# Performance work log

Measured on AMD Instinct MI355X. Metric: run time of the kernel, lower is better.

The kernel has to match this reference:

```python
import jax, jax.numpy as jnp
import numpy as np

# Static config derived from img size 144 (min spatial dim > 128 branch):
SCALES = [9, 18, 36]            # kernel sizes (cubic)
WEIGHTS = [0.1, 0.3, 0.6]       # kernel weight ratios
DILATIONS = [2, 2, 2]
STRIDES = [max((k + 1) // 4, 1) for k in SCALES]  # [2, 4, 9]
EPS = 1e-5


def _box_sum(x, k, stride, dil):
    # Local sum over a dilated k^3 window, valid padding (matches F.conv3d
    # with an all-ones [1,1,k,k,k] kernel).
    kern = jnp.ones((1, 1, k, k, k), dtype=x.dtype)
    return jax.lax.conv_general_dilated(
        x, kern,
        window_strides=(stride,) * 3,
        padding='VALID',
        rhs_dilation=(dil,) * 3,
        dimension_numbers=('NCDHW', 'OIDHW', 'NCDHW'))


def setup_inputs() -> dict:
    key = jax.random.key(0)
    k1, k2 = jax.random.split(key)
    shape = (4, 1, 144, 144, 144)
    return {
        'input': jax.random.normal(k1, shape, dtype=jnp.float32),
        'target': jax.random.normal(k2, shape, dtype=jnp.float32),
    }


def reference(input, target):
    B = input.shape[0]
    input_2 = input * input
    target_2 = target * target
    input_target = input * target
    lncc_total = jnp.float32(0.0)
    for k, w, dil, st in zip(SCALES, WEIGHTS, DILATIONS, STRIDES):
        i_sum = _box_sum(input, k, st, dil).reshape(B, -1)
        t_sum = _box_sum(target, k, st, dil).reshape(B, -1)
        i2_sum = _box_sum(input_2, k, st, dil).reshape(B, -1)
        t2_sum = _box_sum(target_2, k, st, dil).reshape(B, -1)
        it_sum = _box_sum(input_target, k, st, dil).reshape(B, -1)
        numel = float(k ** 3)
        i_mean = i_sum / numel
        t_mean = t_sum / numel
        cross = it_sum - t_mean * i_sum - i_mean * t_sum + t_mean * i_mean * numel
        i_var = i2_sum - 2.0 * i_mean * i_sum + i_mean * i_mean * numel
        t_var = t2_sum - 2.0 * t_mean * t_sum + t_mean * t_mean * numel
        lncc = (cross * cross) / (i_var * t_var + EPS)
        lncc_total = lncc_total + w * (1.0 - lncc.mean())
    return lncc_total * B
```

## Files before the change

kernel.cpp:

```cpp
#include <hip/hip_runtime.h>


constexpr int BATCH = 4;
constexpr int DIM   = 144;
constexpr int NROWS = BATCH * DIM * DIM;
constexpr float EPS = 1e-5f;

constexpr int N1C  = NROWS * 9;
constexpr int N2Ae = BATCH * 72 * 64 * 64;
constexpr int N2Be = BATCH * 72 * 28 * 28;
constexpr int N2C  = BATCH * DIM * 9 * 9;


__device__ __forceinline__ float lncc_val(const float s[5], float inv_numel) {
    float cross = s[4] - s[0] * s[1] * inv_numel;
    float ivar  = s[2] - s[0] * s[0] * inv_numel;
    float tvar  = s[3] - s[1] * s[1] * inv_numel;
    return (cross * cross) / (ivar * tvar + EPS);
}

__device__ __forceinline__ void block_reduce_store(float acc, float* slot) {
    #pragma unroll
    for (int off = 32; off > 0; off >>= 1) acc += __shfl_down(acc, off, 64);
    __shared__ float sm[4];
    int lane = threadIdx.x & 63, wid = threadIdx.x >> 6;
    if (lane == 0) sm[wid] = acc;
    __syncthreads();
    if (threadIdx.x == 0) *slot = sm[0] + sm[1] + sm[2] + sm[3];
}


__device__ void aXY_body(int blk, const float* __restrict__ in,
                         const float* __restrict__ tg,
                         float* __restrict__ b2a, float* xs)
{
    const int p  = blk >> 2;
    const int c  = blk & 3;
    const int b  = p / 72;
    const int ez = p % 72;
    const int xo0 = c * 16;
    const size_t gpl = (size_t)(b * DIM + 2 * ez) * (DIM * DIM);
    const int t = threadIdx.x;

    for (int i = t; i < 576; i += 256) {
        int yp = i >> 3, dp = i & 7;
        int dx0 = dp * 2;
        int e0  = xo0 + dx0;
        const float* rowa = in + gpl + (size_t)(2 * yp) * DIM;
        const float* rowb = tg + gpl + (size_t)(2 * yp) * DIM;
        const float4* ga = (const float4*)rowa + (e0 >> 1);
        const float4* gb = (const float4*)rowb + (e0 >> 1);
        float ea[10], eb[10];
        #pragma unroll
        for (int k = 0; k < 5; ++k) {
            float4 A = ga[k]; ea[2 * k] = A.x; ea[2 * k + 1] = A.z;
            float4 B = gb[k]; eb[2 * k] = B.x; eb[2 * k + 1] = B.z;
        }
        float* xr = &xs[yp * 82 + dx0];
        #pragma unroll
        for (int q = 0; q < 5; ++q) {
            float2 sq; sq.x = 0.f; sq.y = 0.f;
            #pragma unroll
            for (int j = 0; j < 9; ++j) {
                float a0 = ea[j],     b0 = eb[j];
                float a1 = ea[j + 1], b1 = eb[j + 1];
                float v0, v1;
                if (q == 0)      { v0 = a0;      v1 = a1; }
                else if (q == 1) { v0 = b0;      v1 = b1; }
                else if (q == 2) { v0 = a0 * a0; v1 = a1 * a1; }
                else if (q == 3) { v0 = b0 * b0; v1 = b1 * b1; }
                else             { v0 = a0 * b0; v1 = a1 * b1; }
                sq.x += v0; sq.y += v1;
            }
            *(float2*)&xr[q * 16] = sq;
        }
    }
    __syncthreads();

    if (t < 160) {
        int dp = t & 7;
        int ch = (t >> 3) & 3;
        int q  = t >> 5;
        int dx0 = 2 * dp, yo0 = ch * 16;
        const float2* xp2 = (const float2*)xs + ((q * 16 + dx0) >> 1);
        float2 s; s.x = 0.f; s.y = 0.f;
        #pragma unroll
        for (int j = 0; j < 9; ++j) {
            float2 v = xp2[(yo0 + j) * 41];
            s.x += v.x; s.y += v.y;
        }
        float2* ob = (float2*)(b2a + (size_t)q * N2Ae
                               + ((size_t)p * 64 + yo0) * 64 + xo0 + dx0);
        ob[0] = s;
        #pragma unroll
        for (int i2 = 1; i2 < 16; ++i2) {
            float2 vn = xp2[(yo0 + i2 + 8) * 41];
            float2 vo = xp2[(yo0 + i2 - 1) * 41];
            s.x += vn.x - vo.x; s.y += vn.y - vo.y;
            ob[(size_t)i2 * 32] = s;
        }
    }
}

constexpr int CXROWS   = 24;
constexpr int CXSTRIDE = 292;

__device__ void cX_body(int blk, const float* __restrict__ in,
                        const float* __restrict__ tg,
                        float* __restrict__ b1c, float* lv)
{
    const int t = threadIdx.x;
    const int row0 = blk * CXROWS;
    const float4* gin = (const float4*)(in + (size_t)row0 * DIM);
    const float4* gtg = (const float4*)(tg + (size_t)row0 * DIM);
    for (int i4 = t; i4 < CXROWS * 36; i4 += 256) {
        int rr = i4 / 36, k = i4 % 36;
        float4 A = gin[i4], B = gtg[i4];
        float4* d = (float4*)&lv[rr * CXSTRIDE + k * 8];
        float4 w0; w0.x = A.x; w0.y = B.x; w0.z = A.y; w0.w = B.y;
        float4 w1; w1.x = A.z; w1.y = B.z; w1.z = A.w; w1.w = B.w;
        d[0] = w0; d[1] = w1;
    }
    __syncthreads();
    if (t < CXROWS * 9) {
        int rr = t / 9, xo = t % 9;
        const float2* pp = (const float2*)&lv[rr * CXSTRIDE] + xo * 9;
        float s0 = 0.f, s1 = 0.f, s2 = 0.f, s3 = 0.f, s4 = 0.f;
        #pragma unroll
        for (int j = 0; j < 36; ++j) {
            float2 ab = pp[2 * j];
            float a = ab.x, bb = ab.y;
            s0 += a; s1 += bb; s2 += a * a; s3 += bb * bb; s4 += a * bb;
        }
        int o = (row0 + rr) * 9 + xo;
        b1c[o] = s0; b1c[N1C + o] = s1; b1c[2 * N1C + o] = s2;
        b1c[3 * N1C + o] = s3; b1c[4 * N1C + o] = s4;
    }
}

constexpr int B_AXY = BATCH * 72 * 4;
constexpr int B_CX  = NROWS / CXROWS;
constexpr int SM1   = CXROWS * CXSTRIDE;

__global__ __launch_bounds__(256) void k1(const float* __restrict__ in,
                                          const float* __restrict__ tg,
                                          float* __restrict__ b2a,
                                          float* __restrict__ b1c)
{
    __shared__ float smem[SM1];
    int blk = blockIdx.x;
    if (blk < B_AXY) aXY_body(blk, in, tg, b2a, smem);
    else             cX_body(blk - B_AXY, in, tg, b1c, smem);
}


__device__ __forceinline__ void bXY_body(int tid, const float* __restrict__ b2a,
                                         float* __restrict__ b2b)
{
    const int total = BATCH * 72 * 28 * 14;
    if (tid >= total) return;
    int px = tid % 14;
    int yo = (tid / 14) % 28;
    int p  = tid / 392;
    const float* ib = b2a + (size_t)p * 4096;
    int r0 = 2 * yo * 64, r1 = r0 + 9 * 64;
    #pragma unroll
    for (int q = 0; q < 5; ++q) {
        const float* pq = ib + (size_t)q * N2Ae;
        const float4* row0 = (const float4*)(pq + r0);
        const float4* row1 = (const float4*)(pq + r1);
        float4 a0 = row0[px], b0 = row0[px + 2];
        float4 a1 = row1[px], b1 = row1[px + 2];
        float2 o;
        o.x = a0.x + b0.y + a1.x + b1.y;
        o.y = a0.z + b0.w + a1.z + b1.w;
        *(float2*)(b2b + (size_t)q * N2Be + (size_t)p * 784 + yo * 28 + 2 * px) = o;
    }
}

__device__ __forceinline__ void cY_body(int tid, const float* __restrict__ b1c,
                                        float* __restrict__ b2c)
{
    const int total = BATCH * DIM * 9 * 9 * 8;
    if (tid >= total) return;
    int sp   = tid & 7;
    int rest = tid >> 3;
    int xo = rest % 9;
    int yo = (rest / 9) % 9;
    int bz = rest / 81;
    const float* base = b1c + (size_t)bz * DIM * 9 + xo;

    float s[5] = {0.f, 0.f, 0.f, 0.f, 0.f};
    #pragma unroll
    for (int j = 0; j < 36; ++j) {
        if ((j & 7) == sp) {
            int y = 9 * yo + 2 * j;
            #pragma unroll
            for (int q = 0; q < 5; ++q) s[q] += base[(size_t)q * N1C + y * 9];
        }
    }
    #pragma unroll
    for (int off = 1; off < 8; off <<= 1) {
        #pragma unroll
        for (int q = 0; q < 5; ++q) s[q] += __shfl_xor(s[q], off, 64);
    }
    if (sp == 0) {
        float* ob = b2c + (size_t)bz * 81 + yo * 9 + xo;
        #pragma unroll
        for (int q = 0; q < 5; ++q) ob[(size_t)q * N2C] = s[q];
    }
}

constexpr int B_BXY = (BATCH * 72 * 28 * 14) / 256;
constexpr int B_CY  = (BATCH * DIM * 9 * 9 * 8) / 256;

__global__ __launch_bounds__(256) void k2a(const float* __restrict__ b2a,
                                           const float* __restrict__ b1c,
                                           float* __restrict__ b2b,
                                           float* __restrict__ b2c)
{
    int blk = blockIdx.x;
    if (blk < B_BXY) bXY_body(blk * 256 + threadIdx.x, b2a, b2b);
    else             cY_body((blk - B_BXY) * 256 + threadIdx.x, b1c, b2c);
}


__device__ __forceinline__ void aZ_body(int blk, const float* __restrict__ b2a,
                                        float* __restrict__ pA)
{
    int tid = blk * 256 + threadIdx.x;
    float acc = 0.f;
    {
        int xo = tid & 63;
        int yo = (tid >> 6) & 63;
        int ch = (tid >> 12) & 7;
        int b  = tid >> 15;
        const int zo0 = ch * 8;
        const int OO = 64 * 64;
        const float* base = b2a + (size_t)b * 72 * OO + yo * 64 + xo;

        float s[5] = {0.f, 0.f, 0.f, 0.f, 0.f};
        #pragma unroll
        for (int j = 0; j < 9; ++j) {
            #pragma unroll
            for (int q = 0; q < 5; ++q)
                s[q] += base[(size_t)q * N2Ae + (zo0 + j) * OO];
        }
        acc += lncc_val(s, 1.0f / 729.0f);
        #pragma unroll
        for (int i = 1; i < 8; ++i) {
            #pragma unroll
            for (int q = 0; q < 5; ++q)
                s[q] += base[(size_t)q * N2Ae + (zo0 + i + 8) * OO]
                      - base[(size_t)q * N2Ae + (zo0 + i - 1) * OO];
            acc += lncc_val(s, 1.0f / 729.0f);
        }
    }
    block_reduce_store(acc, pA + blk);
}

__device__ __forceinline__ void bZ_body(int blk, const float* __restrict__ b2b,
                                        float* __restrict__ pB)
{
    int tid = blk * 256 + threadIdx.x;
    float acc = 0.f;
    {
        int sp   = tid & 7;
        int rest = tid >> 3;
        int px = rest % 14;
        int yo = (rest / 14) % 28;
        int zo = (rest / 392) % 28;
        int b  = rest / 10976;
        const int OO = 784;
        const float* base = b2b + (size_t)b * 72 * OO + yo * 28 + 2 * px;

        float sx[5] = {0.f, 0.f, 0.f, 0.f, 0.f};
        float sy[5] = {0.f, 0.f, 0.f, 0.f, 0.f};
        #pragma unroll
        for (int j = 0; j < 18; ++j) {
            if ((j & 7) == sp) {
                #pragma unroll
                for (int q = 0; q < 5; ++q) {
                    float2 v = *(const float2*)(base + (size_t)q * N2Be
                                                + (2 * zo + j) * OO);
                    sx[q] += v.x; sy[q] += v.y;
                }
            }
        }
        #pragma unroll
        for (int off = 1; off < 8; off <<= 1) {
            #pragma unroll
            for (int q = 0; q < 5; ++q) {
                sx[q] += __shfl_xor(sx[q], off, 64);
                sy[q] += __shfl_xor(sy[q], off, 64);
            }
        }
        if (sp == 0)
            acc = lncc_val(sx, 1.0f / 5832.0f) + lncc_val(sy, 1.0f / 5832.0f);
    }
    block_reduce_store(acc, pB + blk);
}

__device__ __forceinline__ void cZ_body(int blk, const float* __restrict__ b2c,
                                        float* __restrict__ pC)
{
    int tid = blk * 256 + threadIdx.x;
    const int total = BATCH * 9 * 9 * 9 * 16;
    float acc = 0.f;
    if (tid < total) {
        int sp   = tid & 15;
        int rest = tid >> 4;
        int xo = rest % 9;
        int yo = (rest / 9) % 9;
        int zo = (rest / 81) % 9;
        int b  = rest / 729;
        const int OO = 81;
        const float* base = b2c + (size_t)b * DIM * OO + yo * 9 + xo;

        float s[5] = {0.f, 0.f, 0.f, 0.f, 0.f};
        #pragma unroll
        for (int j = 0; j < 36; ++j) {
            if ((j & 15) == sp) {
                int z = 9 * zo + 2 * j;
                #pragma unroll
                for (int q = 0; q < 5; ++q) s[q] += base[(size_t)q * N2C + z * OO];
            }
        }
        #pragma unroll
        for (int off = 1; off < 16; off <<= 1) {
            #pragma unroll
            for (int q = 0; q < 5; ++q) s[q] += __shfl_xor(s[q], off, 64);
        }
        if (sp == 0) acc = lncc_val(s, 1.0f / 46656.0f);
    }
    block_reduce_store(acc, pC + blk);
}

constexpr int B_AZ = (BATCH * 8 * 64 * 64) / 256;
constexpr int B_BZ = (BATCH * 28 * 28 * 14 * 8) / 256;
constexpr int B_CZ = (BATCH * 9 * 9 * 9 * 16 + 255) / 256;

__global__ __launch_bounds__(256) void k2b(const float* __restrict__ b2a,
                                           const float* __restrict__ b2b,
                                           const float* __restrict__ b2c,
                                           float* __restrict__ pA,
                                           float* __restrict__ pB,
                                           float* __restrict__ pC)
{
    int blk = blockIdx.x;
    if (blk < B_AZ)             aZ_body(blk, b2a, pA);
    else if (blk < B_AZ + B_BZ) bZ_body(blk - B_AZ, b2b, pB);
    else                        cZ_body(blk - B_AZ - B_BZ, b2c, pC);
}


__global__ __launch_bounds__(256) void k4(const float* __restrict__ pA,
                                          const float* __restrict__ pB,
                                          const float* __restrict__ pC,
                                          float* __restrict__ out)
{
    const int t = threadIdx.x;
    float sA = 0.f, sB = 0.f, sC = 0.f;
    for (int i = t; i < B_AZ; i += 256) sA += pA[i];
    for (int i = t; i < B_BZ; i += 256) sB += pB[i];
    for (int i = t; i < B_CZ; i += 256) sC += pC[i];
    float s = (0.1f / 262144.0f) * sA + (0.3f / 21952.0f) * sB
            + (0.6f / 729.0f) * sC;
    #pragma unroll
    for (int off = 32; off > 0; off >>= 1) s += __shfl_down(s, off, 64);
    __shared__ float sm[4];
    int lane = t & 63, wid = t >> 6;
    if (lane == 0) sm[wid] = s;
    __syncthreads();
    if (t == 0) out[0] = 4.0f - (sm[0] + sm[1] + sm[2] + sm[3]);
}

extern "C" void kernel_launch(void* const* d_in, const int* in_sizes, int n_in,
                              void* d_out, int out_size, void* d_ws, size_t ws_size,
                              hipStream_t stream) {
    const float* input  = (const float*)d_in[0];
    const float* target = (const float*)d_in[1];
    float* out = (float*)d_out;

    float* b2a = (float*)d_ws;
    float* b1c = b2a + (size_t)5 * N2Ae;
    float* b2b = b1c + (size_t)5 * N1C;
    float* b2c = b2b + (size_t)5 * N2Be;
    float* pA  = b2c + (size_t)5 * N2C;
    float* pB  = pA + B_AZ;
    float* pC  = pB + B_BZ;

    k1<<<B_AXY + B_CX, 256, 0, stream>>>(input, target, b2a, b1c);
    k2a<<<B_BXY + B_CY, 256, 0, stream>>>(b2a, b1c, b2b, b2c);
    k2b<<<B_AZ + B_BZ + B_CZ, 256, 0, stream>>>(b2a, b2b, b2c, pA, pB, pC);
    k4<<<1, 256, 0, stream>>>(pA, pB, pC, out);
}
```

Measured before the change: 88.10 us.

## Fuse scale-C X and Y passes per plane and regroup stages across kernels

```diff
diff --git a/kernel.cpp b/kernel.cpp
--- a/kernel.cpp
+++ b/kernel.cpp
@@ -3,10 +3,8 @@
 
 constexpr int BATCH = 4;
 constexpr int DIM   = 144;
-constexpr int NROWS = BATCH * DIM * DIM;
 constexpr float EPS = 1e-5f;
 
-constexpr int N1C  = NROWS * 9;
 constexpr int N2Ae = BATCH * 72 * 64 * 64;
 constexpr int N2Be = BATCH * 72 * 28 * 28;
 constexpr int N2C  = BATCH * DIM * 9 * 9;
@@ -102,57 +100,94 @@
     }
 }
 
-constexpr int CXROWS   = 24;
-constexpr int CXSTRIDE = 292;
-
-__device__ void cX_body(int blk, const float* __restrict__ in,
-                        const float* __restrict__ tg,
-                        float* __restrict__ b1c, float* lv)
-{
+
+__device__ void cXY_body(int blk, const float* __restrict__ in,
+                         const float* __restrict__ tg,
+                         float* __restrict__ b2c, float* xs)
+{
+    const size_t gpl = (size_t)blk * (DIM * DIM);
     const int t = threadIdx.x;
-    const int row0 = blk * CXROWS;
-    const float4* gin = (const float4*)(in + (size_t)row0 * DIM);
-    const float4* gtg = (const float4*)(tg + (size_t)row0 * DIM);
-    for (int i4 = t; i4 < CXROWS * 36; i4 += 256) {
-        int rr = i4 / 36, k = i4 % 36;
-        float4 A = gin[i4], B = gtg[i4];
-        float4* d = (float4*)&lv[rr * CXSTRIDE + k * 8];
-        float4 w0; w0.x = A.x; w0.y = B.x; w0.z = A.y; w0.w = B.y;
-        float4 w1; w1.x = A.z; w1.y = B.z; w1.z = A.w; w1.w = B.w;
-        d[0] = w0; d[1] = w1;
+
+    for (int i = t; i < 144 * 9; i += 256) {
+        int y = i / 9, xo = i % 9;
+        int x0 = 9 * xo;
+        const float2* ra = (const float2*)(in + gpl + (size_t)y * DIM) + (x0 >> 1);
+        const float2* rb = (const float2*)(tg + gpl + (size_t)y * DIM) + (x0 >> 1);
+        const bool odd = (x0 & 1) != 0;
+        float s0 = 0.f, s1 = 0.f, s2 = 0.f, s3 = 0.f, s4 = 0.f;
+        #pragma unroll
+        for (int j = 0; j < 36; ++j) {
+            float2 va = ra[j], vb = rb[j];
+            float a  = odd ? va.y : va.x;
+            float bb = odd ? vb.y : vb.x;
+            s0 += a; s1 += bb; s2 += a * a; s3 += bb * bb; s4 += a * bb;
+        }
+        float* d = &xs[y * 48 + xo * 5];
+        d[0] = s0; d[1] = s1; d[2] = s2; d[3] = s3; d[4] = s4;
     }
     __syncthreads();
-    if (t < CXROWS * 9) {
-        int rr = t / 9, xo = t % 9;
-        const float2* pp = (const float2*)&lv[rr * CXSTRIDE] + xo * 9;
-        float s0 = 0.f, s1 = 0.f, s2 = 0.f, s3 = 0.f, s4 = 0.f;
-        #pragma unroll
-        for (int j = 0; j < 36; ++j) {
-            float2 ab = pp[2 * j];
-            float a = ab.x, bb = ab.y;
-            s0 += a; s1 += bb; s2 += a * a; s3 += bb * bb; s4 += a * bb;
-        }
-        int o = (row0 + rr) * 9 + xo;
-        b1c[o] = s0; b1c[N1C + o] = s1; b1c[2 * N1C + o] = s2;
-        b1c[3 * N1C + o] = s3; b1c[4 * N1C + o] = s4;
+
+    for (int i = t; i < 405; i += 256) {
+        int q  = i % 5;
+        int xo = (i / 5) % 9;
+        int yo = i / 45;
+        float s = 0.f;
+        #pragma unroll
+        for (int j = 0; j < 36; ++j)
+            s += xs[(9 * yo + 2 * j) * 48 + xo * 5 + q];
+        b2c[(size_t)q * N2C + ((size_t)blk * 9 + yo) * 9 + xo] = s;
     }
 }
 
 constexpr int B_AXY = BATCH * 72 * 4;
-constexpr int B_CX  = NROWS / CXROWS;
-constexpr int SM1   = CXROWS * CXSTRIDE;
+constexpr int B_CXY = BATCH * DIM;
+constexpr int SM1   = 144 * 48;
 
 __global__ __launch_bounds__(256) void k1(const float* __restrict__ in,
                                           const float* __restrict__ tg,
                                           float* __restrict__ b2a,
-                                          float* __restrict__ b1c)
+                                          float* __restrict__ b2c)
 {
     __shared__ float smem[SM1];
     int blk = blockIdx.x;
     if (blk < B_AXY) aXY_body(blk, in, tg, b2a, smem);
-    else             cX_body(blk - B_AXY, in, tg, b1c, smem);
-}
-
+    else             cXY_body(blk - B_AXY, in, tg, b2c, smem);
+}
+
+
+__device__ __forceinline__ void aZ_body(int blk, const float* __restrict__ b2a,
+                                        float* __restrict__ pA)
+{
+    int tid = blk * 256 + threadIdx.x;
+    float acc = 0.f;
+    {
+        int xo = tid & 63;
+        int yo = (tid >> 6) & 63;
+        int ch = (tid >> 12) & 15;
+        int b  = tid >> 16;
+        const int zo0 = ch * 4;
+        const int OO = 64 * 64;
+        const float* base = b2a + (size_t)b * 72 * OO + yo * 64 + xo;
+
+        float s[5] = {0.f, 0.f, 0.f, 0.f, 0.f};
+        #pragma unroll
+        for (int j = 0; j < 9; ++j) {
+            #pragma unroll
+            for (int q = 0; q < 5; ++q)
+                s[q] += base[(size_t)q * N2Ae + (zo0 + j) * OO];
+        }
+        acc += lncc_val(s, 1.0f / 729.0f);
+        #pragma unroll
+        for (int i = 1; i < 4; ++i) {
+            #pragma unroll
+            for (int q = 0; q < 5; ++q)
+                s[q] += base[(size_t)q * N2Ae + (zo0 + i + 8) * OO]
+                      - base[(size_t)q * N2Ae + (zo0 + i - 1) * OO];
+            acc += lncc_val(s, 1.0f / 729.0f);
+        }
+    }
+    block_reduce_store(acc, pA + blk);
+}
 
 __device__ __forceinline__ void bXY_body(int tid, const float* __restrict__ b2a,
                                          float* __restrict__ b2b)
@@ -178,129 +213,6 @@
     }
 }
 
-__device__ __forceinline__ void cY_body(int tid, const float* __restrict__ b1c,
-                                        float* __restrict__ b2c)
-{
-    const int total = BATCH * DIM * 9 * 9 * 8;
-    if (tid >= total) return;
-    int sp   = tid & 7;
-    int rest = tid >> 3;
-    int xo = rest % 9;
-    int yo = (rest / 9) % 9;
-    int bz = rest / 81;
-    const float* base = b1c + (size_t)bz * DIM * 9 + xo;
-
-    float s[5] = {0.f, 0.f, 0.f, 0.f, 0.f};
-    #pragma unroll
-    for (int j = 0; j < 36; ++j) {
-        if ((j & 7) == sp) {
-            int y = 9 * yo + 2 * j;
-            #pragma unroll
-            for (int q = 0; q < 5; ++q) s[q] += base[(size_t)q * N1C + y * 9];
-        }
-    }
-    #pragma unroll
-    for (int off = 1; off < 8; off <<= 1) {
-        #pragma unroll
-        for (int q = 0; q < 5; ++q) s[q] += __shfl_xor(s[q], off, 64);
-    }
-    if (sp == 0) {
-        float* ob = b2c + (size_t)bz * 81 + yo * 9 + xo;
-        #pragma unroll
-        for (int q = 0; q < 5; ++q) ob[(size_t)q * N2C] = s[q];
-    }
-}
-
-constexpr int B_BXY = (BATCH * 72 * 28 * 14) / 256;
-constexpr int B_CY  = (BATCH * DIM * 9 * 9 * 8) / 256;
-
-__global__ __launch_bounds__(256) void k2a(const float* __restrict__ b2a,
-                                           const float* __restrict__ b1c,
-                                           float* __restrict__ b2b,
-                                           float* __restrict__ b2c)
-{
-    int blk = blockIdx.x;
-    if (blk < B_BXY) bXY_body(blk * 256 + threadIdx.x, b2a, b2b);
-    else             cY_body((blk - B_BXY) * 256 + threadIdx.x, b1c, b2c);
-}
-
-
-__device__ __forceinline__ void aZ_body(int blk, const float* __restrict__ b2a,
-                                        float* __restrict__ pA)
-{
-    int tid = blk * 256 + threadIdx.x;
-    float acc = 0.f;
-    {
-        int xo = tid & 63;
-        int yo = (tid >> 6) & 63;
-        int ch = (tid >> 12) & 7;
-        int b  = tid >> 15;
-        const int zo0 = ch * 8;
-        const int OO = 64 * 64;
-        const float* base = b2a + (size_t)b * 72 * OO + yo * 64 + xo;
-
-        float s[5] = {0.f, 0.f, 0.f, 0.f, 0.f};
-        #pragma unroll
-        for (int j = 0; j < 9; ++j) {
-            #pragma unroll
-            for (int q = 0; q < 5; ++q)
-                s[q] += base[(size_t)q * N2Ae + (zo0 + j) * OO];
-        }
-        acc += lncc_val(s, 1.0f / 729.0f);
-        #pragma unroll
-        for (int i = 1; i < 8; ++i) {
-            #pragma unroll
-            for (int q = 0; q < 5; ++q)
-                s[q] += base[(size_t)q * N2Ae + (zo0 + i + 8) * OO]
-                      - base[(size_t)q * N2Ae + (zo0 + i - 1) * OO];
-            acc += lncc_val(s, 1.0f / 729.0f);
-        }
-    }
-    block_reduce_store(acc, pA + blk);
-}
-
-__device__ __forceinline__ void bZ_body(int blk, const float* __restrict__ b2b,
-                                        float* __restrict__ pB)
-{
-    int tid = blk * 256 + threadIdx.x;
-    float acc = 0.f;
-    {
-        int sp   = tid & 7;
-        int rest = tid >> 3;
-        int px = rest % 14;
-        int yo = (rest / 14) % 28;
-        int zo = (rest / 392) % 28;
-        int b  = rest / 10976;
-        const int OO = 784;
-        const float* base = b2b + (size_t)b * 72 * OO + yo * 28 + 2 * px;
-
-        float sx[5] = {0.f, 0.f, 0.f, 0.f, 0.f};
-        float sy[5] = {0.f, 0.f, 0.f, 0.f, 0.f};
-        #pragma unroll
-        for (int j = 0; j < 18; ++j) {
-            if ((j & 7) == sp) {
-                #pragma unroll
-                for (int q = 0; q < 5; ++q) {
-                    float2 v = *(const float2*)(base + (size_t)q * N2Be
-                                                + (2 * zo + j) * OO);
-                    sx[q] += v.x; sy[q] += v.y;
-                }
-            }
-        }
-        #pragma unroll
-        for (int off = 1; off < 8; off <<= 1) {
-            #pragma unroll
-            for (int q = 0; q < 5; ++q) {
-                sx[q] += __shfl_xor(sx[q], off, 64);
-                sy[q] += __shfl_xor(sy[q], off, 64);
-            }
-        }
-        if (sp == 0)
-            acc = lncc_val(sx, 1.0f / 5832.0f) + lncc_val(sy, 1.0f / 5832.0f);
-    }
-    block_reduce_store(acc, pB + blk);
-}
-
 __device__ __forceinline__ void cZ_body(int blk, const float* __restrict__ b2c,
                                         float* __restrict__ pC)
 {
@@ -336,21 +248,71 @@
     block_reduce_store(acc, pC + blk);
 }
 
-constexpr int B_AZ = (BATCH * 8 * 64 * 64) / 256;
+constexpr int B_AZ  = (BATCH * 16 * 64 * 64) / 256;
+constexpr int B_BXY = (BATCH * 72 * 28 * 14) / 256;
+constexpr int B_CZ  = (BATCH * 9 * 9 * 9 * 16 + 255) / 256;
+
+__global__ __launch_bounds__(256) void k2(const float* __restrict__ b2a,
+                                          const float* __restrict__ b2c,
+                                          float* __restrict__ b2b,
+                                          float* __restrict__ pA,
+                                          float* __restrict__ pC)
+{
+    int blk = blockIdx.x;
+    if (blk < B_AZ)              aZ_body(blk, b2a, pA);
+    else if (blk < B_AZ + B_BXY) bXY_body((blk - B_AZ) * 256 + threadIdx.x, b2a, b2b);
+    else                         cZ_body(blk - B_AZ - B_BXY, b2c, pC);
+}
+
+
+__device__ __forceinline__ void bZ_body(int blk, const float* __restrict__ b2b,
+                                        float* __restrict__ pB)
+{
+    int tid = blk * 256 + threadIdx.x;
+    float acc = 0.f;
+    {
+        int sp   = tid & 7;
+        int rest = tid >> 3;
+        int px = rest % 14;
+        int yo = (rest / 14) % 28;
+        int zo = (rest / 392) % 28;
+        int b  = rest / 10976;
+        const int OO = 784;
+        const float* base = b2b + (size_t)b * 72 * OO + yo * 28 + 2 * px;
+
+        float sx[5] = {0.f, 0.f, 0.f, 0.f, 0.f};
+        float sy[5] = {0.f, 0.f, 0.f, 0.f, 0.f};
+        #pragma unroll
+        for (int j = 0; j < 18; ++j) {
+            if ((j & 7) == sp) {
+                #pragma unroll
+                for (int q = 0; q < 5; ++q) {
+                    float2 v = *(const float2*)(base + (size_t)q * N2Be
+                                                + (2 * zo + j) * OO);
+                    sx[q] += v.x; sy[q] += v.y;
+                }
+            }
+        }
+        #pragma unroll
+        for (int off = 1; off < 8; off <<= 1) {
+            #pragma unroll
+            for (int q = 0; q < 5; ++q) {
+                sx[q] += __shfl_xor(sx[q], off, 64);
+                sy[q] += __shfl_xor(sy[q], off, 64);
+            }
+        }
+        if (sp == 0)
+            acc = lncc_val(sx, 1.0f / 5832.0f) + lncc_val(sy, 1.0f / 5832.0f);
+    }
+    block_reduce_store(acc, pB + blk);
+}
+
 constexpr int B_BZ = (BATCH * 28 * 28 * 14 * 8) / 256;
-constexpr int B_CZ = (BATCH * 9 * 9 * 9 * 16 + 255) / 256;
-
-__global__ __launch_bounds__(256) void k2b(const float* __restrict__ b2a,
-                                           const float* __restrict__ b2b,
-                                           const float* __restrict__ b2c,
-                                           float* __restrict__ pA,
-                                           float* __restrict__ pB,
-                                           float* __restrict__ pC)
-{
-    int blk = blockIdx.x;
-    if (blk < B_AZ)             aZ_body(blk, b2a, pA);
-    else if (blk < B_AZ + B_BZ) bZ_body(blk - B_AZ, b2b, pB);
-    else                        cZ_body(blk - B_AZ - B_BZ, b2c, pC);
+
+__global__ __launch_bounds__(256) void k3(const float* __restrict__ b2b,
+                                          float* __restrict__ pB)
+{
+    bZ_body(blockIdx.x, b2b, pB);
 }
 
 
@@ -383,15 +345,14 @@
     float* out = (float*)d_out;
 
     float* b2a = (float*)d_ws;
-    float* b1c = b2a + (size_t)5 * N2Ae;
-    float* b2b = b1c + (size_t)5 * N1C;
+    float* b2b = b2a + (size_t)5 * N2Ae;
     float* b2c = b2b + (size_t)5 * N2Be;
     float* pA  = b2c + (size_t)5 * N2C;
     float* pB  = pA + B_AZ;
     float* pC  = pB + B_BZ;
 
-    k1<<<B_AXY + B_CX, 256, 0, stream>>>(input, target, b2a, b1c);
-    k2a<<<B_BXY + B_CY, 256, 0, stream>>>(b2a, b1c, b2b, b2c);
-    k2b<<<B_AZ + B_BZ + B_CZ, 256, 0, stream>>>(b2a, b2b, b2c, pA, pB, pC);
+    k1<<<B_AXY + B_CXY, 256, 0, stream>>>(input, target, b2a, b2c);
+    k2<<<B_AZ + B_BXY + B_CZ, 256, 0, stream>>>(b2a, b2c, b2b, pA, pC);
+    k3<<<B_BZ, 256, 0, stream>>>(b2b, pB);
     k4<<<1, 256, 0, stream>>>(pA, pB, pC, out);
 }
```

After: 99.47 us. 12.9% more time.

## Move scale-A z-pass into second kernel and stage cY through LDS

Applied to the files above, without the earlier changes.

```diff
diff --git a/kernel.cpp b/kernel.cpp
--- a/kernel.cpp
+++ b/kernel.cpp
@@ -153,6 +153,40 @@
     else             cX_body(blk - B_AXY, in, tg, b1c, smem);
 }
 
+
+__device__ __forceinline__ void aZ_body(int blk, const float* __restrict__ b2a,
+                                        float* __restrict__ pA)
+{
+    int tid = blk * 256 + threadIdx.x;
+    float acc = 0.f;
+    {
+        int xo = tid & 63;
+        int yo = (tid >> 6) & 63;
+        int ch = (tid >> 12) & 3;
+        int b  = tid >> 14;
+        const int zo0 = ch * 16;
+        const int OO = 64 * 64;
+        const float* base = b2a + (size_t)b * 72 * OO + yo * 64 + xo;
+
+        float s[5] = {0.f, 0.f, 0.f, 0.f, 0.f};
+        #pragma unroll
+        for (int j = 0; j < 9; ++j) {
+            #pragma unroll
+            for (int q = 0; q < 5; ++q)
+                s[q] += base[(size_t)q * N2Ae + (zo0 + j) * OO];
+        }
+        acc += lncc_val(s, 1.0f / 729.0f);
+        #pragma unroll
+        for (int i = 1; i < 16; ++i) {
+            #pragma unroll
+            for (int q = 0; q < 5; ++q)
+                s[q] += base[(size_t)q * N2Ae + (zo0 + i + 8) * OO]
+                      - base[(size_t)q * N2Ae + (zo0 + i - 1) * OO];
+            acc += lncc_val(s, 1.0f / 729.0f);
+        }
+    }
+    block_reduce_store(acc, pA + blk);
+}
 
 __device__ __forceinline__ void bXY_body(int tid, const float* __restrict__ b2a,
                                          float* __restrict__ b2b)
@@ -178,86 +212,48 @@
     }
 }
 
-__device__ __forceinline__ void cY_body(int tid, const float* __restrict__ b1c,
-                                        float* __restrict__ b2c)
-{
-    const int total = BATCH * DIM * 9 * 9 * 8;
-    if (tid >= total) return;
-    int sp   = tid & 7;
-    int rest = tid >> 3;
-    int xo = rest % 9;
-    int yo = (rest / 9) % 9;
-    int bz = rest / 81;
-    const float* base = b1c + (size_t)bz * DIM * 9 + xo;
-
-    float s[5] = {0.f, 0.f, 0.f, 0.f, 0.f};
+__device__ void cYL_body(int blk, const float* __restrict__ b1c,
+                         float* __restrict__ b2c, float* lds)
+{
+    const int t = threadIdx.x;
     #pragma unroll
-    for (int j = 0; j < 36; ++j) {
-        if ((j & 7) == sp) {
-            int y = 9 * yo + 2 * j;
-            #pragma unroll
-            for (int q = 0; q < 5; ++q) s[q] += base[(size_t)q * N1C + y * 9];
-        }
-    }
-    #pragma unroll
-    for (int off = 1; off < 8; off <<= 1) {
-        #pragma unroll
-        for (int q = 0; q < 5; ++q) s[q] += __shfl_xor(s[q], off, 64);
-    }
-    if (sp == 0) {
-        float* ob = b2c + (size_t)bz * 81 + yo * 9 + xo;
-        #pragma unroll
-        for (int q = 0; q < 5; ++q) ob[(size_t)q * N2C] = s[q];
-    }
-}
-
+    for (int q = 0; q < 5; ++q) {
+        const float4* src = (const float4*)(b1c + (size_t)q * N1C
+                                            + (size_t)blk * 1296);
+        float4* dst = (float4*)(lds + q * 1296);
+        for (int i = t; i < 324; i += 256) dst[i] = src[i];
+    }
+    __syncthreads();
+    for (int i = t; i < 405; i += 256) {
+        int q  = i % 5;
+        int xo = (i / 5) % 9;
+        int yo = i / 45;
+        const float* base = lds + q * 1296 + xo;
+        float s = 0.f;
+        #pragma unroll
+        for (int j = 0; j < 36; ++j) s += base[(9 * yo + 2 * j) * 9];
+        b2c[(size_t)q * N2C + ((size_t)blk * 9 + yo) * 9 + xo] = s;
+    }
+}
+
+constexpr int B_AZ  = (BATCH * 4 * 64 * 64) / 256;
 constexpr int B_BXY = (BATCH * 72 * 28 * 14) / 256;
-constexpr int B_CY  = (BATCH * DIM * 9 * 9 * 8) / 256;
-
-__global__ __launch_bounds__(256) void k2a(const float* __restrict__ b2a,
-                                           const float* __restrict__ b1c,
-                                           float* __restrict__ b2b,
-                                           float* __restrict__ b2c)
-{
+constexpr int B_CYL = BATCH * DIM;
+constexpr int SM2   = 5 * 1296;
+
+__global__ __launch_bounds__(256) void k2(const float* __restrict__ b2a,
+                                          const float* __restrict__ b1c,
+                                          float* __restrict__ b2b,
+                                          float* __restrict__ b2c,
+                                          float* __restrict__ pA)
+{
+    __shared__ float smem[SM2];
     int blk = blockIdx.x;
-    if (blk < B_BXY) bXY_body(blk * 256 + threadIdx.x, b2a, b2b);
-    else             cY_body((blk - B_BXY) * 256 + threadIdx.x, b1c, b2c);
-}
-
-
-__device__ __forceinline__ void aZ_body(int blk, const float* __restrict__ b2a,
-                                        float* __restrict__ pA)
-{
-    int tid = blk * 256 + threadIdx.x;
-    float acc = 0.f;
-    {
-        int xo = tid & 63;
-        int yo = (tid >> 6) & 63;
-        int ch = (tid >> 12) & 7;
-        int b  = tid >> 15;
-        const int zo0 = ch * 8;
-        const int OO = 64 * 64;
-        const float* base = b2a + (size_t)b * 72 * OO + yo * 64 + xo;
-
-        float s[5] = {0.f, 0.f, 0.f, 0.f, 0.f};
-        #pragma unroll
-        for (int j = 0; j < 9; ++j) {
-            #pragma unroll
-            for (int q = 0; q < 5; ++q)
-                s[q] += base[(size_t)q * N2Ae + (zo0 + j) * OO];
-        }
-        acc += lncc_val(s, 1.0f / 729.0f);
-        #pragma unroll
-        for (int i = 1; i < 8; ++i) {
-            #pragma unroll
-            for (int q = 0; q < 5; ++q)
-                s[q] += base[(size_t)q * N2Ae + (zo0 + i + 8) * OO]
-                      - base[(size_t)q * N2Ae + (zo0 + i - 1) * OO];
-            acc += lncc_val(s, 1.0f / 729.0f);
-        }
-    }
-    block_reduce_store(acc, pA + blk);
-}
+    if (blk < B_AZ)              aZ_body(blk, b2a, pA);
+    else if (blk < B_AZ + B_BXY) bXY_body((blk - B_AZ) * 256 + threadIdx.x, b2a, b2b);
+    else                         cYL_body(blk - B_AZ - B_BXY, b1c, b2c, smem);
+}
+
 
 __device__ __forceinline__ void bZ_body(int blk, const float* __restrict__ b2b,
                                         float* __restrict__ pB)
@@ -336,21 +332,17 @@
     block_reduce_store(acc, pC + blk);
 }
 
-constexpr int B_AZ = (BATCH * 8 * 64 * 64) / 256;
 constexpr int B_BZ = (BATCH * 28 * 28 * 14 * 8) / 256;
 constexpr int B_CZ = (BATCH * 9 * 9 * 9 * 16 + 255) / 256;
 
-__global__ __launch_bounds__(256) void k2b(const float* __restrict__ b2a,
-                                           const float* __restrict__ b2b,
-                                           const float* __restrict__ b2c,
-                                           float* __restrict__ pA,
-                                           float* __restrict__ pB,
-                                           float* __restrict__ pC)
+__global__ __launch_bounds__(256) void k3(const float* __restrict__ b2b,
+                                          const float* __restrict__ b2c,
+                                          float* __restrict__ pB,
+                                          float* __restrict__ pC)
 {
     int blk = blockIdx.x;
-    if (blk < B_AZ)             aZ_body(blk, b2a, pA);
-    else if (blk < B_AZ + B_BZ) bZ_body(blk - B_AZ, b2b, pB);
-    else                        cZ_body(blk - B_AZ - B_BZ, b2c, pC);
+    if (blk < B_BZ) bZ_body(blk, b2b, pB);
+    else            cZ_body(blk - B_BZ, b2c, pC);
 }
 
 
@@ -391,7 +383,7 @@
     float* pC  = pB + B_BZ;
 
     k1<<<B_AXY + B_CX, 256, 0, stream>>>(input, target, b2a, b1c);
-    k2a<<<B_BXY + B_CY, 256, 0, stream>>>(b2a, b1c, b2b, b2c);
-    k2b<<<B_AZ + B_BZ + B_CZ, 256, 0, stream>>>(b2a, b2b, b2c, pA, pB, pC);
+    k2<<<B_AZ + B_BXY + B_CYL, 256, 0, stream>>>(b2a, b1c, b2b, b2c, pA);
+    k3<<<B_BZ + B_CZ, 256, 0, stream>>>(b2b, b2c, pB, pC);
     k4<<<1, 256, 0, stream>>>(pA, pB, pC, out);
 }
```

New measurement: 77.83 us (median of 3 runs). -11.7%, faster.
